# Kernel optimization log

Measured on AMD Instinct MI355X. Metric: run time of the kernel, lower is better.

## Reference

```python
import jax, jax.numpy as jnp
import numpy as np

B, D_IN, D_HID, D_OUT = 16384, 512, 512, 512
E, K = 8, 2
VQ_COEFF, LB_COEFF = 0.05, 0.01
LOG100 = float(np.log(100.0))
LOG2 = float(np.log(2.0))


def _normalize(v):
    # torch F.normalize(dim=1): x / max(||x||, 1e-12)
    n = jnp.linalg.norm(v, axis=-1, keepdims=True)
    return v / jnp.maximum(n, 1e-12)


def _cv_squared(v):
    # torch .var() is unbiased (ddof=1)
    return jnp.var(v, ddof=1) / (jnp.mean(v) ** 2 + 1e-10)


def _rbm_layer(x, rm, W, b, ca, temp):
    # x: [B, d_in], rm: [E, d_in], W: [E, d_out, d_in], b: [E, d_out]
    rm_n = jax.lax.stop_gradient(_normalize(rm))          # .detach() in source
    nx = _normalize(x)
    dists = nx @ rm_n.T                                    # [B, E]
    top_v, top_i = jax.lax.top_k(dists, K)                 # [B, K]
    tv = jax.nn.softmax(top_v, axis=-1)                    # softmax over top-k
    bsz = dists.shape[0]
    attn = jnp.zeros_like(dists).at[jnp.arange(bsz)[:, None], top_i].set(tv)
    # const_attention is frozen (requires_grad=False)
    inp_att = jnp.exp(jnp.minimum(jax.lax.stop_gradient(ca), LOG100))  # [E]
    # dense gather-compute-scatter: expert e output for every token, masked by attn
    eo = jnp.einsum('bi,eoi->beo', x, W) * inp_att[None, :, None] + b[None, :, :]
    out = jnp.einsum('be,beo->bo', jax.lax.stop_gradient(attn), eo)    # att.detach()
    out = out * jnp.exp(jnp.minimum(temp, LOG100))
    # aux losses (eval mode: no EMA memory update)
    vq = -(nx[:, None, :] * rm_n[top_i]).sum(-1)           # [B, K]
    vq_loss = (tv * vq).sum(-1).mean()
    lb = _cv_squared(attn.sum(0))
    aux = VQ_COEFF * vq_loss + LB_COEFF * lb               # sim_coeff = 0
    return out, aux


def setup_inputs() -> dict:
    key = jax.random.key(0)
    ks = jax.random.split(key, 8)
    x = jax.random.normal(ks[0], (B, D_IN), dtype=jnp.float32)
    rm0 = _normalize(jax.random.normal(ks[1], (E, D_IN), dtype=jnp.float32))
    W0 = jax.random.normal(ks[2], (E, D_HID, D_IN), dtype=jnp.float32) / np.sqrt(D_IN)
    b0 = jnp.zeros((E, D_HID), dtype=jnp.float32)
    rm1 = _normalize(jax.random.normal(ks[3], (E, D_HID), dtype=jnp.float32))
    W1 = jax.random.normal(ks[4], (E, D_OUT, D_HID), dtype=jnp.float32) / np.sqrt(D_HID)
    b1 = jnp.zeros((E, D_OUT), dtype=jnp.float32)
    temp0 = jnp.full((1,), LOG2, dtype=jnp.float32)
    temp1 = jnp.full((1,), LOG2, dtype=jnp.float32)
    ca0 = jnp.zeros((E,), dtype=jnp.float32)
    ca1 = jnp.zeros((E,), dtype=jnp.float32)
    return {"x": x, "rm0": rm0, "W0": W0, "b0": b0, "temp0": temp0, "ca0": ca0,
            "rm1": rm1, "W1": W1, "b1": b1, "temp1": temp1, "ca1": ca1}


def reference(x, rm0, W0, b0, temp0, ca0, rm1, W1, b1, temp1, ca1):
    h0, a0 = _rbm_layer(x, rm0, W0, b0, ca0, temp0)
    h_emb = h0                      # embedding tapped after layer 0 (pre-activation)
    h = jax.nn.relu(h0)             # norm_type=None -> no norm
    h1, a1 = _rbm_layer(h, rm1, W1, b1, ca1, temp1)
    return (h_emb, h1, a0 + a1)
```

## Files before the change

kernel.cpp:

```cpp
#include <hip/hip_runtime.h>
#include <cmath>
#include <cstdint>

#define NTOK   16384
#define DM     512
#define NEXP   8
#define LOG100 4.605170185988092f

typedef _Float16 half8  __attribute__((ext_vector_type(8)));
typedef _Float16 half4  __attribute__((ext_vector_type(4)));
typedef float    floatx4 __attribute__((ext_vector_type(4)));

#define MFMA_F16(a, b, c) __builtin_amdgcn_mfma_f32_16x16x32_f16((a), (b), (c), 0, 0, 0)

__device__ __forceinline__ void gl_lds16(const void* g, void* l) {
    __builtin_amdgcn_global_load_lds(
        (const __attribute__((address_space(1))) void*)g,
        (__attribute__((address_space(3))) void*)l, 16, 0, 0);
}


__global__ __launch_bounds__(256) void prep_kernel(
    const float* __restrict__ rm0, const float* __restrict__ rm1,
    const float* __restrict__ ca0, const float* __restrict__ ca1,
    const float* __restrict__ temp0, const float* __restrict__ temp1,
    float* __restrict__ ctrl, float* __restrict__ rmn)
{
    int tid = threadIdx.x, lane = tid & 63, w = tid >> 6;
    if (tid < 32) ((int*)ctrl)[tid] = 0;
    if (tid >= 32 && tid < 48) ctrl[tid] = 0.f;
    if (tid == 48 || tid == 49) ctrl[tid] = 0.f;
    if (tid == 50) ctrl[50] = expf(fminf(temp0[0], LOG100));
    if (tid == 51) ctrl[51] = expf(fminf(temp1[0], LOG100));
    if (tid >= 52 && tid < 68) {
        int i = tid - 52;
        ctrl[tid] = expf(fminf(i < 8 ? ca0[i] : ca1[i - 8], LOG100));
    }
    for (int r = w; r < 16; r += 4) {
        const float* src = (r < 8) ? (rm0 + r * DM) : (rm1 + (r - 8) * DM);
        float v[8]; float ss = 0.f;
        #pragma unroll
        for (int j = 0; j < 8; ++j) { v[j] = src[lane + 64 * j]; ss += v[j] * v[j]; }
        #pragma unroll
        for (int off = 32; off > 0; off >>= 1) ss += __shfl_xor(ss, off);
        float inv = 1.f / fmaxf(sqrtf(ss), 1e-12f);
        float* dst = rmn + r * DM;
        #pragma unroll
        for (int j = 0; j < 8; ++j) dst[lane + 64 * j] = v[j] * inv;
    }
}

__global__ __launch_bounds__(256) void conv_w_kernel(
    const float4* __restrict__ W0, const float4* __restrict__ W1,
    half4* __restrict__ w0hi, half4* __restrict__ w0lo, half4* __restrict__ w1h)
{
    int i = blockIdx.x * 256 + threadIdx.x;
    float4 a = W0[i], b = W1[i];
    const float* ap = (const float*)&a;
    const float* bp = (const float*)&b;
    half4 hi, lo, h1;
    #pragma unroll
    for (int j = 0; j < 4; ++j) {
        _Float16 h = (_Float16)ap[j];
        hi[j] = h;
        lo[j] = (_Float16)(ap[j] - (float)h);
        h1[j] = (_Float16)bp[j];
    }
    w0hi[i] = hi; w0lo[i] = lo; w1h[i] = h1;
}

__global__ __launch_bounds__(256) void route_kernel(
    const float* __restrict__ src,
    const float* __restrict__ rmn,
    int relu_in,
    _Float16* __restrict__ dst_hi,
    _Float16* __restrict__ dst_lo,
    float* __restrict__ zbase,
    unsigned char* __restrict__ key,
    float2* __restrict__ wts,
    float2* __restrict__ bs)
{
    __shared__ float rmLds[NEXP * DM];
    int tid = threadIdx.x;
    for (int i = tid; i < NEXP * DM; i += 256) rmLds[i] = rmn[i];
    __syncthreads();
    int lane = tid & 63, w = tid >> 6;
    int token = blockIdx.x * 4 + w;

    const float* row = src + (size_t)token * DM;
    float x[8]; float ss = 0.f;
    #pragma unroll
    for (int j = 0; j < 8; ++j) {
        float v = row[lane + 64 * j];
        if (relu_in) v = fmaxf(v, 0.f);
        x[j] = v; ss += v * v;
    }
    #pragma unroll
    for (int j = 0; j < 8; ++j) {
        _Float16 h = (_Float16)x[j];
        dst_hi[(size_t)token * DM + lane + 64 * j] = h;
        if (dst_lo) dst_lo[(size_t)token * DM + lane + 64 * j] = (_Float16)(x[j] - (float)h);
    }
    {
        float4 z = make_float4(0.f, 0.f, 0.f, 0.f);
        float4* zr = (float4*)(zbase + (size_t)token * DM);
        zr[lane * 2] = z;
        zr[lane * 2 + 1] = z;
    }
    float d[8];
    #pragma unroll
    for (int e = 0; e < 8; ++e) {
        float a = 0.f;
        #pragma unroll
        for (int j = 0; j < 8; ++j) a += x[j] * rmLds[e * DM + lane + 64 * j];
        d[e] = a;
    }
    #pragma unroll
    for (int off = 32; off > 0; off >>= 1) {
        ss += __shfl_xor(ss, off);
        #pragma unroll
        for (int e = 0; e < 8; ++e) d[e] += __shfl_xor(d[e], off);
    }
    float inv = 1.f / fmaxf(sqrtf(ss), 1e-12f);
    float best = -1e30f, second = -1e30f; int be = 0, se = 0;
    #pragma unroll
    for (int e = 0; e < 8; ++e) {
        float de = d[e] * inv;
        if (de > best)        { second = best; se = be; best = de; be = e; }
        else if (de > second) { second = de; se = e; }
    }
    float z = expf(second - best);
    float w0 = 1.f / (1.f + z), w1 = z / (1.f + z);
    if (lane == 0) {
        key[token] = (unsigned char)be;
        key[NTOK + token] = (unsigned char)se;
        wts[token] = make_float2(w0, w1);
        bs[token] = make_float2(best, second);
    }
}

__global__ __launch_bounds__(256) void compact_kernel(
    const unsigned char* __restrict__ key,
    const float2* __restrict__ wts,
    const float2* __restrict__ bs,
    int* __restrict__ cnt,
    unsigned short* __restrict__ bkt,
    float* __restrict__ imp,
    float* __restrict__ vq_acc)
{
    int slot = blockIdx.x >> 3, e = blockIdx.x & 7;
    const unsigned char* k = key + slot * NTOK;
    unsigned short* ob = bkt + (size_t)(slot * 8 + e) * NTOK;
    __shared__ int wc[2][4];
    int tid = threadIdx.x, lane = tid & 63, w = tid >> 6;
    int base = 0;
    float wsum = 0.f, vqs = 0.f;
    for (int c = 0; c < 64; ++c) {
        int tok = c * 256 + tid;
        bool m = (k[tok] == (unsigned char)e);
        unsigned long long mask = __ballot(m);
        int p = c & 1;
        if (lane == 0) wc[p][w] = __popcll(mask);
        __syncthreads();
        int off = base;
        for (int i = 0; i < w; ++i) off += wc[p][i];
        if (m) {
            int pre = __popcll(mask & ((1ull << lane) - 1ull));
            ob[off + pre] = (unsigned short)tok;
            float2 wp = wts[tok]; float2 b2 = bs[tok];
            float wv = slot ? wp.y : wp.x;
            wsum += wv;
            vqs  += wv * (slot ? b2.y : b2.x);
        }
        base += wc[p][0] + wc[p][1] + wc[p][2] + wc[p][3];
    }
    #pragma unroll
    for (int off = 32; off > 0; off >>= 1) {
        wsum += __shfl_xor(wsum, off);
        vqs  += __shfl_xor(vqs, off);
    }
    __shared__ float rw[4], rv[4];
    if (lane == 0) { rw[w] = wsum; rv[w] = vqs; }
    __syncthreads();
    if (tid == 0) {
        cnt[slot * 8 + e] = base;
        float W = rw[0] + rw[1] + rw[2] + rw[3];
        float V = rv[0] + rv[1] + rv[2] + rv[3];
        atomicAdd(&imp[e], W);
        atomicAdd(vq_acc, -V);
    }
}

template <bool SPLIT>
__global__ __launch_bounds__(256) void gemm_kernel(
    const _Float16* __restrict__ Ahi, const _Float16* __restrict__ Alo,
    const _Float16* __restrict__ Whi, const _Float16* __restrict__ Wlo,
    const float* __restrict__ bias,
    const float* __restrict__ iav,
    const float* __restrict__ tscp,
    const int* __restrict__ cnt,
    const unsigned short* __restrict__ bkt,
    const float2* __restrict__ wts,
    float* __restrict__ outp)
{
    __shared__ __align__(16) _Float16 lds[2 * 128 * 64];
    __shared__ int tokLds[128];
    _Float16* tA = lds;
    _Float16* tB = lds + 128 * 64;

    int bx = blockIdx.x;
    int e = bx & 7; int r = bx >> 3;
    int n0 = (r & 3) << 7; r >>= 2;
    int slot = r & 1; int mt = r >> 1;
    int M = cnt[slot * 8 + e];
    int m0 = mt << 7;
    if (m0 >= M) return;
    int valid = min(128, M - m0);
    int tid = threadIdx.x, lane = tid & 63, w = tid >> 6;
    const unsigned short* ob = bkt + (size_t)(slot * 8 + e) * NTOK;
    if (tid < 128) tokLds[tid] = ob[m0 + min(tid, valid - 1)];
    __syncthreads();

    floatx4 acc[4][4];
    #pragma unroll
    for (int mi = 0; mi < 4; ++mi)
        #pragma unroll
        for (int ni = 0; ni < 4; ++ni) acc[mi][ni] = (floatx4){0.f, 0.f, 0.f, 0.f};

    const _Float16* WbH = Whi + ((size_t)e * DM + n0) * DM;
    const _Float16* WbL = SPLIT ? (Wlo + ((size_t)e * DM + n0) * DM) : nullptr;

    int subRow = lane >> 3, p = lane & 7;
    int cSt = p ^ (subRow & 7);
    int wm = w >> 1, wn = w & 1;
    int r0 = wm * 64, c0 = wn * 64;
    int q = lane >> 4, l15 = lane & 15;

    constexpr int KIT = SPLIT ? 16 : 8;
    constexpr int KSTEP = SPLIT ? 32 : 64;

    const _Float16* aPtr[4]; const _Float16* bPtr[4];
    _Float16* aDst[4]; _Float16* bDst[4];
    #pragma unroll
    for (int jj = 0; jj < 4; ++jj) {
        int j = w + jj * 4;
        int row = j * 8 + subRow;
        int tok = tokLds[row];
        if constexpr (SPLIT) {
            aPtr[jj] = (cSt < 4) ? (Ahi + (size_t)tok * DM + cSt * 8)
                                 : (Alo + (size_t)tok * DM + (cSt - 4) * 8);
            bPtr[jj] = (cSt < 4) ? (WbH + (size_t)row * DM + cSt * 8)
                                 : (WbL + (size_t)row * DM + (cSt - 4) * 8);
        } else {
            aPtr[jj] = Ahi + (size_t)tok * DM + cSt * 8;
            bPtr[jj] = WbH + (size_t)row * DM + cSt * 8;
        }
        aDst[jj] = tA + j * 512;
        bDst[jj] = tB + j * 512;
    }
    const half8 *aHp[4], *aLp[4], *bHp[4], *bLp[4];
    #pragma unroll
    for (int i = 0; i < 4; ++i) {
        int ra = r0 + i * 16 + l15;
        int rb = c0 + i * 16 + l15;
        if constexpr (SPLIT) {
            aHp[i] = (const half8*)(tA + ra * 64 + ((q) ^ (ra & 7)) * 8);
            aLp[i] = (const half8*)(tA + ra * 64 + ((q + 4) ^ (ra & 7)) * 8);
            bHp[i] = (const half8*)(tB + rb * 64 + ((q) ^ (rb & 7)) * 8);
            bLp[i] = (const half8*)(tB + rb * 64 + ((q + 4) ^ (rb & 7)) * 8);
        } else {
            aHp[i] = (const half8*)(tA + ra * 64 + ((q) ^ (ra & 7)) * 8);
            aLp[i] = (const half8*)(tA + ra * 64 + ((4 + q) ^ (ra & 7)) * 8);
            bHp[i] = (const half8*)(tB + rb * 64 + ((q) ^ (rb & 7)) * 8);
            bLp[i] = (const half8*)(tB + rb * 64 + ((4 + q) ^ (rb & 7)) * 8);
        }
    }

    for (int kb = 0; kb < KIT; ++kb) {
        #pragma unroll
        for (int jj = 0; jj < 4; ++jj) {
            gl_lds16(aPtr[jj], (void*)aDst[jj]);
            aPtr[jj] += KSTEP;
        }
        #pragma unroll
        for (int jj = 0; jj < 4; ++jj) {
            gl_lds16(bPtr[jj], (void*)bDst[jj]);
            bPtr[jj] += KSTEP;
        }
        __syncthreads();

        if constexpr (SPLIT) {
            half8 ah[4], al[4];
            #pragma unroll
            for (int mi = 0; mi < 4; ++mi) { ah[mi] = *aHp[mi]; al[mi] = *aLp[mi]; }
            #pragma unroll
            for (int ni = 0; ni < 4; ++ni) {
                half8 bh = *bHp[ni];
                half8 bl = *bLp[ni];
                #pragma unroll
                for (int mi = 0; mi < 4; ++mi) acc[mi][ni] = MFMA_F16(ah[mi], bh, acc[mi][ni]);
                #pragma unroll
                for (int mi = 0; mi < 4; ++mi) acc[mi][ni] = MFMA_F16(ah[mi], bl, acc[mi][ni]);
                #pragma unroll
                for (int mi = 0; mi < 4; ++mi) acc[mi][ni] = MFMA_F16(al[mi], bh, acc[mi][ni]);
            }
        } else {
            half8 a[4];
            #pragma unroll
            for (int mi = 0; mi < 4; ++mi) a[mi] = *aHp[mi];
            #pragma unroll
            for (int ni = 0; ni < 4; ++ni) {
                half8 b = *bHp[ni];
                #pragma unroll
                for (int mi = 0; mi < 4; ++mi) acc[mi][ni] = MFMA_F16(a[mi], b, acc[mi][ni]);
            }
            #pragma unroll
            for (int mi = 0; mi < 4; ++mi) a[mi] = *aLp[mi];
            #pragma unroll
            for (int ni = 0; ni < 4; ++ni) {
                half8 b = *bLp[ni];
                #pragma unroll
                for (int mi = 0; mi < 4; ++mi) acc[mi][ni] = MFMA_F16(a[mi], b, acc[mi][ni]);
            }
        }
        __syncthreads();
    }

    float t = *tscp, iae = iav[e];
    float bv[4];
    #pragma unroll
    for (int ni = 0; ni < 4; ++ni) bv[ni] = bias[e * DM + n0 + c0 + ni * 16 + l15];
    #pragma unroll
    for (int mi = 0; mi < 4; ++mi) {
        int liBase = r0 + mi * 16 + q * 4;
        #pragma unroll
        for (int reg = 0; reg < 4; ++reg) {
            int li = liBase + reg;
            if (li < valid) {
                int tok = tokLds[li];
                float2 wp = wts[tok];
                float wgt = slot ? wp.y : wp.x;
                float sg = t * wgt * iae, sb = t * wgt;
                float* orow = outp + (size_t)tok * DM + n0;
                #pragma unroll
                for (int ni = 0; ni < 4; ++ni) {
                    float v = acc[mi][ni][reg] * sg + bv[ni] * sb;
                    int c = c0 + ni * 16 + l15;
                    unsafeAtomicAdd(&orow[c], v);
                }
            }
        }
    }
}

__global__ void finalize_kernel(const float* __restrict__ ctrl, float* __restrict__ outp)
{
    if (threadIdx.x == 0) {
        float aux = 0.f;
        for (int l = 0; l < 2; ++l) {
            float vq = ctrl[48 + l] / (float)NTOK;
            float mean = 0.f;
            for (int e = 0; e < 8; ++e) mean += ctrl[32 + l * 8 + e];
            mean *= 0.125f;
            float s = 0.f;
            for (int e = 0; e < 8; ++e) {
                float d = ctrl[32 + l * 8 + e] - mean;
                s += d * d;
            }
            float var = s / 7.f;
            float lb = var / (mean * mean + 1e-10f);
            aux += 0.05f * vq + 0.01f * lb;
        }
        *outp = aux;
    }
}

extern "C" void kernel_launch(void* const* d_in, const int* in_sizes, int n_in,
                              void* d_out, int out_size, void* d_ws, size_t ws_size,
                              hipStream_t stream) {
    const float* x     = (const float*)d_in[0];
    const float* rm0   = (const float*)d_in[1];
    const float* W0    = (const float*)d_in[2];
    const float* b0    = (const float*)d_in[3];
    const float* temp0 = (const float*)d_in[4];
    const float* ca0   = (const float*)d_in[5];
    const float* rm1   = (const float*)d_in[6];
    const float* W1    = (const float*)d_in[7];
    const float* b1    = (const float*)d_in[8];
    const float* temp1 = (const float*)d_in[9];
    const float* ca1   = (const float*)d_in[10];
    float* out = (float*)d_out;

    char* ws = (char*)d_ws;
    float* ctrl = (float*)ws;
    int*   cnt  = (int*)ctrl;
    float* imp  = ctrl + 32;
    float* vq   = ctrl + 48;
    float* tsc  = ctrl + 50;
    float* ia   = ctrl + 52;
    float* rmn  = ctrl + 128;
    float2*        wts = (float2*)(ws + (size_t)64  * 1024);
    float2*        bs  = (float2*)(ws + (size_t)384 * 1024);
    unsigned char* key = (unsigned char*)(ws + (size_t)704 * 1024);

    char* big = ws + (1 << 20);
    half4*          w0hi4 = (half4*)(big);
    half4*          w0lo4 = (half4*)(big + (size_t)4  * 1024 * 1024);
    half4*          w1h4  = (half4*)(big + (size_t)8  * 1024 * 1024);
    _Float16*       w0hi  = (_Float16*)w0hi4;
    _Float16*       w0lo  = (_Float16*)w0lo4;
    _Float16*       w1h   = (_Float16*)w1h4;
    _Float16*       h16   = (_Float16*)(big + (size_t)12 * 1024 * 1024);
    unsigned short* bkt   = (unsigned short*)(big + (size_t)28 * 1024 * 1024);

    _Float16* xhi = (_Float16*)(out + (size_t)NTOK * DM);
    _Float16* xlo = xhi + (size_t)NTOK * DM;
    float* h0 = out;
    float* h1 = out + (size_t)NTOK * DM;

    prep_kernel<<<1, 256, 0, stream>>>(rm0, rm1, ca0, ca1, temp0, temp1, ctrl, rmn);
    conv_w_kernel<<<2048, 256, 0, stream>>>((const float4*)W0, (const float4*)W1,
                                            w0hi4, w0lo4, w1h4);

    route_kernel<<<4096, 256, 0, stream>>>(x, rmn, 0, xhi, xlo, h0,
        key, wts, bs);
    compact_kernel<<<16, 256, 0, stream>>>(key, wts, bs, cnt, bkt, imp, vq);
    gemm_kernel<true><<<8192, 256, 0, stream>>>(xhi, xlo, w0hi, w0lo, b0, ia, tsc,
        cnt, bkt, wts, h0);

    route_kernel<<<4096, 256, 0, stream>>>(h0, rmn + 4096, 1, h16, (_Float16*)nullptr, h1,
        key + 2 * NTOK, wts + NTOK, bs + NTOK);
    compact_kernel<<<16, 256, 0, stream>>>(key + 2 * NTOK, wts + NTOK, bs + NTOK,
        cnt + 16, bkt + 16 * NTOK, imp + 8, vq + 1);
    gemm_kernel<false><<<8192, 256, 0, stream>>>(h16, (const _Float16*)nullptr, w1h,
        (const _Float16*)nullptr, b1, ia + 8, tsc + 1,
        cnt + 16, bkt + 16 * NTOK, wts + NTOK, h1);

    finalize_kernel<<<1, 64, 0, stream>>>(ctrl, out + (size_t)2 * NTOK * DM);
}
```

Measured before the change: 509.4 us.

## Fuse fp16 conversion into gathered GEMMs and replace atomics with slot-separated stores

The first routing kernel no longer writes fp16 hi/lo copies of x or zero-fills the output. The layer-0 GEMM now loads fp32 token rows directly, splits them into hi/lo halves in registers, and writes each top-k slot's result to its own buffer with plain stores. The second routing pass sums the two slot buffers into the embedding output and applies relu in the same pass. The layer-1 GEMM converts relu'd fp32 input on the fly and runs as two ordered launches, one per slot, with the second accumulating non-atomically. Tiles shrink from 128x128 to 64x64, which means many more blocks and more redundant weight reloads, in exchange for removing the atomic-add traffic and the intermediate fp16 buffers.

```diff
diff --git a/kernel.cpp b/kernel.cpp
--- a/kernel.cpp
+++ b/kernel.cpp
@@ -69,16 +69,9 @@
     w0hi[i] = hi; w0lo[i] = lo; w1h[i] = h1;
 }
 
-__global__ __launch_bounds__(256) void route_kernel(
-    const float* __restrict__ src,
-    const float* __restrict__ rmn,
-    int relu_in,
-    _Float16* __restrict__ dst_hi,
-    _Float16* __restrict__ dst_lo,
-    float* __restrict__ zbase,
-    unsigned char* __restrict__ key,
-    float2* __restrict__ wts,
-    float2* __restrict__ bs)
+__global__ __launch_bounds__(256) void route0_kernel(
+    const float* __restrict__ src, const float* __restrict__ rmn,
+    unsigned char* __restrict__ key, float2* __restrict__ wts, float2* __restrict__ bs)
 {
     __shared__ float rmLds[NEXP * DM];
     int tid = threadIdx.x;
@@ -90,23 +83,7 @@
     const float* row = src + (size_t)token * DM;
     float x[8]; float ss = 0.f;
     #pragma unroll
-    for (int j = 0; j < 8; ++j) {
-        float v = row[lane + 64 * j];
-        if (relu_in) v = fmaxf(v, 0.f);
-        x[j] = v; ss += v * v;
-    }
-    #pragma unroll
-    for (int j = 0; j < 8; ++j) {
-        _Float16 h = (_Float16)x[j];
-        dst_hi[(size_t)token * DM + lane + 64 * j] = h;
-        if (dst_lo) dst_lo[(size_t)token * DM + lane + 64 * j] = (_Float16)(x[j] - (float)h);
-    }
-    {
-        float4 z = make_float4(0.f, 0.f, 0.f, 0.f);
-        float4* zr = (float4*)(zbase + (size_t)token * DM);
-        zr[lane * 2] = z;
-        zr[lane * 2 + 1] = z;
-    }
+    for (int j = 0; j < 8; ++j) { float v = row[lane + 64 * j]; x[j] = v; ss += v * v; }
     float d[8];
     #pragma unroll
     for (int e = 0; e < 8; ++e) {
@@ -139,14 +116,63 @@
     }
 }
 
+__global__ __launch_bounds__(256) void route1_kernel(
+    const float* s0, const float* s1, float* hemb,
+    const float* __restrict__ rmn,
+    unsigned char* __restrict__ key, float2* __restrict__ wts, float2* __restrict__ bs)
+{
+    __shared__ float rmLds[NEXP * DM];
+    int tid = threadIdx.x;
+    for (int i = tid; i < NEXP * DM; i += 256) rmLds[i] = rmn[i];
+    __syncthreads();
+    int lane = tid & 63, w = tid >> 6;
+    int token = blockIdx.x * 4 + w;
+
+    float x[8]; float ss = 0.f;
+    #pragma unroll
+    for (int j = 0; j < 8; ++j) {
+        size_t idx = (size_t)token * DM + lane + 64 * j;
+        float v = s0[idx] + s1[idx];
+        hemb[idx] = v;
+        float r = fmaxf(v, 0.f);
+        x[j] = r; ss += r * r;
+    }
+    float d[8];
+    #pragma unroll
+    for (int e = 0; e < 8; ++e) {
+        float a = 0.f;
+        #pragma unroll
+        for (int j = 0; j < 8; ++j) a += x[j] * rmLds[e * DM + lane + 64 * j];
+        d[e] = a;
+    }
+    #pragma unroll
+    for (int off = 32; off > 0; off >>= 1) {
+        ss += __shfl_xor(ss, off);
+        #pragma unroll
+        for (int e = 0; e < 8; ++e) d[e] += __shfl_xor(d[e], off);
+    }
+    float inv = 1.f / fmaxf(sqrtf(ss), 1e-12f);
+    float best = -1e30f, second = -1e30f; int be = 0, se = 0;
+    #pragma unroll
+    for (int e = 0; e < 8; ++e) {
+        float de = d[e] * inv;
+        if (de > best)        { second = best; se = be; best = de; be = e; }
+        else if (de > second) { second = de; se = e; }
+    }
+    float z = expf(second - best);
+    float w0 = 1.f / (1.f + z), w1 = z / (1.f + z);
+    if (lane == 0) {
+        key[token] = (unsigned char)be;
+        key[NTOK + token] = (unsigned char)se;
+        wts[token] = make_float2(w0, w1);
+        bs[token] = make_float2(best, second);
+    }
+}
+
 __global__ __launch_bounds__(256) void compact_kernel(
-    const unsigned char* __restrict__ key,
-    const float2* __restrict__ wts,
-    const float2* __restrict__ bs,
-    int* __restrict__ cnt,
-    unsigned short* __restrict__ bkt,
-    float* __restrict__ imp,
-    float* __restrict__ vq_acc)
+    const unsigned char* __restrict__ key, const float2* __restrict__ wts,
+    const float2* __restrict__ bs, int* __restrict__ cnt,
+    unsigned short* __restrict__ bkt, float* __restrict__ imp, float* __restrict__ vq_acc)
 {
     int slot = blockIdx.x >> 3, e = blockIdx.x & 7;
     const unsigned char* k = key + slot * NTOK;
@@ -184,154 +210,247 @@
     __syncthreads();
     if (tid == 0) {
         cnt[slot * 8 + e] = base;
-        float W = rw[0] + rw[1] + rw[2] + rw[3];
-        float V = rv[0] + rv[1] + rv[2] + rv[3];
-        atomicAdd(&imp[e], W);
-        atomicAdd(vq_acc, -V);
-    }
-}
-
-template <bool SPLIT>
-__global__ __launch_bounds__(256) void gemm_kernel(
-    const _Float16* __restrict__ Ahi, const _Float16* __restrict__ Alo,
+        atomicAdd(&imp[e], rw[0] + rw[1] + rw[2] + rw[3]);
+        atomicAdd(vq_acc, -(rv[0] + rv[1] + rv[2] + rv[3]));
+    }
+}
+
+__global__ __launch_bounds__(256) void gemm0_kernel(
+    const float* __restrict__ x,
     const _Float16* __restrict__ Whi, const _Float16* __restrict__ Wlo,
-    const float* __restrict__ bias,
-    const float* __restrict__ iav,
+    const float* __restrict__ bias, const float* __restrict__ iav,
     const float* __restrict__ tscp,
-    const int* __restrict__ cnt,
-    const unsigned short* __restrict__ bkt,
+    const int* __restrict__ cnt, const unsigned short* __restrict__ bkt,
     const float2* __restrict__ wts,
-    float* __restrict__ outp)
-{
-    __shared__ __align__(16) _Float16 lds[2 * 128 * 64];
-    __shared__ int tokLds[128];
-    _Float16* tA = lds;
-    _Float16* tB = lds + 128 * 64;
+    float* __restrict__ s0, float* __restrict__ s1)
+{
+    __shared__ __align__(16) _Float16 tA[64 * 64];
+    __shared__ __align__(16) _Float16 tB[64 * 64];
+    __shared__ int tokLds[64];
 
     int bx = blockIdx.x;
-    int e = bx & 7; int r = bx >> 3;
-    int n0 = (r & 3) << 7; r >>= 2;
-    int slot = r & 1; int mt = r >> 1;
+    int e = bx & 7, nIdx = (bx >> 3) & 7, slot = (bx >> 6) & 1, mt = bx >> 7;
     int M = cnt[slot * 8 + e];
-    int m0 = mt << 7;
+    int m0 = mt << 6;
     if (m0 >= M) return;
-    int valid = min(128, M - m0);
+    int n0 = nIdx << 6;
+    int valid = min(64, M - m0);
     int tid = threadIdx.x, lane = tid & 63, w = tid >> 6;
     const unsigned short* ob = bkt + (size_t)(slot * 8 + e) * NTOK;
-    if (tid < 128) tokLds[tid] = ob[m0 + min(tid, valid - 1)];
+    if (tid < 64) tokLds[tid] = ob[m0 + min(tid, valid - 1)];
     __syncthreads();
 
-    floatx4 acc[4][4];
-    #pragma unroll
-    for (int mi = 0; mi < 4; ++mi)
-        #pragma unroll
-        for (int ni = 0; ni < 4; ++ni) acc[mi][ni] = (floatx4){0.f, 0.f, 0.f, 0.f};
+    floatx4 acc[2][2];
+    #pragma unroll
+    for (int mi = 0; mi < 2; ++mi)
+        #pragma unroll
+        for (int ni = 0; ni < 2; ++ni) acc[mi][ni] = (floatx4){0.f, 0.f, 0.f, 0.f};
 
     const _Float16* WbH = Whi + ((size_t)e * DM + n0) * DM;
-    const _Float16* WbL = SPLIT ? (Wlo + ((size_t)e * DM + n0) * DM) : nullptr;
+    const _Float16* WbL = Wlo + ((size_t)e * DM + n0) * DM;
 
     int subRow = lane >> 3, p = lane & 7;
     int cSt = p ^ (subRow & 7);
-    int wm = w >> 1, wn = w & 1;
-    int r0 = wm * 64, c0 = wn * 64;
-    int q = lane >> 4, l15 = lane & 15;
-
-    constexpr int KIT = SPLIT ? 16 : 8;
-    constexpr int KSTEP = SPLIT ? 32 : 64;
-
-    const _Float16* aPtr[4]; const _Float16* bPtr[4];
-    _Float16* aDst[4]; _Float16* bDst[4];
-    #pragma unroll
-    for (int jj = 0; jj < 4; ++jj) {
+    const _Float16* bPtr[2]; _Float16* bDst[2];
+    #pragma unroll
+    for (int jj = 0; jj < 2; ++jj) {
         int j = w + jj * 4;
         int row = j * 8 + subRow;
-        int tok = tokLds[row];
-        if constexpr (SPLIT) {
-            aPtr[jj] = (cSt < 4) ? (Ahi + (size_t)tok * DM + cSt * 8)
-                                 : (Alo + (size_t)tok * DM + (cSt - 4) * 8);
-            bPtr[jj] = (cSt < 4) ? (WbH + (size_t)row * DM + cSt * 8)
-                                 : (WbL + (size_t)row * DM + (cSt - 4) * 8);
-        } else {
-            aPtr[jj] = Ahi + (size_t)tok * DM + cSt * 8;
-            bPtr[jj] = WbH + (size_t)row * DM + cSt * 8;
-        }
-        aDst[jj] = tA + j * 512;
+        bPtr[jj] = (cSt < 4) ? (WbH + (size_t)row * DM + cSt * 8)
+                             : (WbL + (size_t)row * DM + (cSt - 4) * 8);
         bDst[jj] = tB + j * 512;
     }
-    const half8 *aHp[4], *aLp[4], *bHp[4], *bLp[4];
-    #pragma unroll
-    for (int i = 0; i < 4; ++i) {
+    int ar = tid >> 2, kc = tid & 3;
+    const float4* aBase = (const float4*)(x + (size_t)tokLds[ar] * DM);
+    _Float16* aDstHi = tA + ar * 64 + ((kc)     ^ (ar & 7)) * 8;
+    _Float16* aDstLo = tA + ar * 64 + ((kc + 4) ^ (ar & 7)) * 8;
+
+    int wm = w >> 1, wn = w & 1;
+    int r0 = wm * 32, c0 = wn * 32;
+    int q = lane >> 4, l15 = lane & 15;
+    const half8 *aHp[2], *aLp[2], *bHp[2], *bLp[2];
+    #pragma unroll
+    for (int i = 0; i < 2; ++i) {
         int ra = r0 + i * 16 + l15;
+        aHp[i] = (const half8*)(tA + ra * 64 + ((q)     ^ (ra & 7)) * 8);
+        aLp[i] = (const half8*)(tA + ra * 64 + ((q + 4) ^ (ra & 7)) * 8);
         int rb = c0 + i * 16 + l15;
-        if constexpr (SPLIT) {
-            aHp[i] = (const half8*)(tA + ra * 64 + ((q) ^ (ra & 7)) * 8);
-            aLp[i] = (const half8*)(tA + ra * 64 + ((q + 4) ^ (ra & 7)) * 8);
-            bHp[i] = (const half8*)(tB + rb * 64 + ((q) ^ (rb & 7)) * 8);
-            bLp[i] = (const half8*)(tB + rb * 64 + ((q + 4) ^ (rb & 7)) * 8);
-        } else {
-            aHp[i] = (const half8*)(tA + ra * 64 + ((q) ^ (ra & 7)) * 8);
-            aLp[i] = (const half8*)(tA + ra * 64 + ((4 + q) ^ (ra & 7)) * 8);
-            bHp[i] = (const half8*)(tB + rb * 64 + ((q) ^ (rb & 7)) * 8);
-            bLp[i] = (const half8*)(tB + rb * 64 + ((4 + q) ^ (rb & 7)) * 8);
-        }
-    }
-
-    for (int kb = 0; kb < KIT; ++kb) {
-        #pragma unroll
-        for (int jj = 0; jj < 4; ++jj) {
-            gl_lds16(aPtr[jj], (void*)aDst[jj]);
-            aPtr[jj] += KSTEP;
-        }
-        #pragma unroll
-        for (int jj = 0; jj < 4; ++jj) {
-            gl_lds16(bPtr[jj], (void*)bDst[jj]);
-            bPtr[jj] += KSTEP;
-        }
+        bHp[i] = (const half8*)(tB + rb * 64 + ((q)     ^ (rb & 7)) * 8);
+        bLp[i] = (const half8*)(tB + rb * 64 + ((q + 4) ^ (rb & 7)) * 8);
+    }
+
+    float4 pf0 = aBase[kc * 2], pf1 = aBase[kc * 2 + 1];
+    for (int kb = 0; kb < 16; ++kb) {
+        float fv[8] = {pf0.x, pf0.y, pf0.z, pf0.w, pf1.x, pf1.y, pf1.z, pf1.w};
+        half8 hi, lo;
+        #pragma unroll
+        for (int j = 0; j < 8; ++j) {
+            _Float16 h = (_Float16)fv[j];
+            hi[j] = h;
+            lo[j] = (_Float16)(fv[j] - (float)h);
+        }
+        *(half8*)aDstHi = hi;
+        *(half8*)aDstLo = lo;
+        gl_lds16(bPtr[0], (void*)bDst[0]);
+        gl_lds16(bPtr[1], (void*)bDst[1]);
+        bPtr[0] += 32; bPtr[1] += 32;
         __syncthreads();
-
-        if constexpr (SPLIT) {
-            half8 ah[4], al[4];
+        if (kb + 1 < 16) {
+            int idx = (kb + 1) * 8 + kc * 2;
+            pf0 = aBase[idx]; pf1 = aBase[idx + 1];
+        }
+        half8 ah[2], al[2];
+        #pragma unroll
+        for (int mi = 0; mi < 2; ++mi) { ah[mi] = *aHp[mi]; al[mi] = *aLp[mi]; }
+        #pragma unroll
+        for (int ni = 0; ni < 2; ++ni) {
+            half8 bh = *bHp[ni];
+            half8 bl = *bLp[ni];
             #pragma unroll
-            for (int mi = 0; mi < 4; ++mi) { ah[mi] = *aHp[mi]; al[mi] = *aLp[mi]; }
+            for (int mi = 0; mi < 2; ++mi) acc[mi][ni] = MFMA_F16(ah[mi], bh, acc[mi][ni]);
             #pragma unroll
-            for (int ni = 0; ni < 4; ++ni) {
-                half8 bh = *bHp[ni];
-                half8 bl = *bLp[ni];
+            for (int mi = 0; mi < 2; ++mi) acc[mi][ni] = MFMA_F16(ah[mi], bl, acc[mi][ni]);
+            #pragma unroll
+            for (int mi = 0; mi < 2; ++mi) acc[mi][ni] = MFMA_F16(al[mi], bh, acc[mi][ni]);
+        }
+        __syncthreads();
+    }
+
+    float* sOut = slot ? s1 : s0;
+    float t = *tscp, iae = iav[e];
+    float bv[2];
+    #pragma unroll
+    for (int ni = 0; ni < 2; ++ni) bv[ni] = bias[e * DM + n0 + c0 + ni * 16 + l15];
+    #pragma unroll
+    for (int mi = 0; mi < 2; ++mi) {
+        int liBase = r0 + mi * 16 + q * 4;
+        #pragma unroll
+        for (int reg = 0; reg < 4; ++reg) {
+            int li = liBase + reg;
+            if (li < valid) {
+                int tok = tokLds[li];
+                float2 wp = wts[tok];
+                float wgt = slot ? wp.y : wp.x;
+                float sg = t * wgt * iae, sb = t * wgt;
+                float* orow = sOut + (size_t)tok * DM + n0;
                 #pragma unroll
-                for (int mi = 0; mi < 4; ++mi) acc[mi][ni] = MFMA_F16(ah[mi], bh, acc[mi][ni]);
-                #pragma unroll
-                for (int mi = 0; mi < 4; ++mi) acc[mi][ni] = MFMA_F16(ah[mi], bl, acc[mi][ni]);
-                #pragma unroll
-                for (int mi = 0; mi < 4; ++mi) acc[mi][ni] = MFMA_F16(al[mi], bh, acc[mi][ni]);
+                for (int ni = 0; ni < 2; ++ni)
+                    orow[c0 + ni * 16 + l15] = acc[mi][ni][reg] * sg + bv[ni] * sb;
             }
-        } else {
-            half8 a[4];
+        }
+    }
+}
+
+__global__ __launch_bounds__(256) void gemm1_kernel(
+    const float* __restrict__ hsrc,
+    const _Float16* __restrict__ Wh,
+    const float* __restrict__ bias, const float* __restrict__ iav,
+    const float* __restrict__ tscp,
+    const int* __restrict__ cnt, const unsigned short* __restrict__ bkt,
+    const float2* __restrict__ wts,
+    int slot, int accum,
+    float* __restrict__ outp)
+{
+    __shared__ __align__(16) _Float16 tA[64 * 64];
+    __shared__ __align__(16) _Float16 tB[64 * 64];
+    __shared__ int tokLds[64];
+
+    int bx = blockIdx.x;
+    int e = bx & 7, nIdx = (bx >> 3) & 7, mt = bx >> 6;
+    int M = cnt[slot * 8 + e];
+    int m0 = mt << 6;
+    if (m0 >= M) return;
+    int n0 = nIdx << 6;
+    int valid = min(64, M - m0);
+    int tid = threadIdx.x, lane = tid & 63, w = tid >> 6;
+    const unsigned short* ob = bkt + (size_t)(slot * 8 + e) * NTOK;
+    if (tid < 64) tokLds[tid] = ob[m0 + min(tid, valid - 1)];
+    __syncthreads();
+
+    floatx4 acc[2][2];
+    #pragma unroll
+    for (int mi = 0; mi < 2; ++mi)
+        #pragma unroll
+        for (int ni = 0; ni < 2; ++ni) acc[mi][ni] = (floatx4){0.f, 0.f, 0.f, 0.f};
+
+    const _Float16* Wb = Wh + ((size_t)e * DM + n0) * DM;
+
+    int subRow = lane >> 3, p = lane & 7;
+    int cSt = p ^ (subRow & 7);
+    const _Float16* bPtr[2]; _Float16* bDst[2];
+    #pragma unroll
+    for (int jj = 0; jj < 2; ++jj) {
+        int j = w + jj * 4;
+        int row = j * 8 + subRow;
+        bPtr[jj] = Wb + (size_t)row * DM + cSt * 8;
+        bDst[jj] = tB + j * 512;
+    }
+    int ar = tid >> 2, kc2 = (tid & 3) * 2;
+    const float4* aBase = (const float4*)(hsrc + (size_t)tokLds[ar] * DM);
+    _Float16* aDst0 = tA + ar * 64 + ((kc2)     ^ (ar & 7)) * 8;
+    _Float16* aDst1 = tA + ar * 64 + ((kc2 + 1) ^ (ar & 7)) * 8;
+
+    int wm = w >> 1, wn = w & 1;
+    int r0 = wm * 32, c0 = wn * 32;
+    int q = lane >> 4, l15 = lane & 15;
+    const half8 *aP0[2], *aP1[2], *bP0[2], *bP1[2];
+    #pragma unroll
+    for (int i = 0; i < 2; ++i) {
+        int ra = r0 + i * 16 + l15;
+        aP0[i] = (const half8*)(tA + ra * 64 + ((q)     ^ (ra & 7)) * 8);
+        aP1[i] = (const half8*)(tA + ra * 64 + ((4 + q) ^ (ra & 7)) * 8);
+        int rb = c0 + i * 16 + l15;
+        bP0[i] = (const half8*)(tB + rb * 64 + ((q)     ^ (rb & 7)) * 8);
+        bP1[i] = (const half8*)(tB + rb * 64 + ((4 + q) ^ (rb & 7)) * 8);
+    }
+
+    float4 pf[4];
+    #pragma unroll
+    for (int j = 0; j < 4; ++j) pf[j] = aBase[kc2 * 2 + j];
+    for (int kb = 0; kb < 8; ++kb) {
+        const float* fp = (const float*)pf;
+        half8 h0v, h1v;
+        #pragma unroll
+        for (int j = 0; j < 8; ++j) h0v[j] = (_Float16)fmaxf(fp[j], 0.f);
+        #pragma unroll
+        for (int j = 0; j < 8; ++j) h1v[j] = (_Float16)fmaxf(fp[8 + j], 0.f);
+        *(half8*)aDst0 = h0v;
+        *(half8*)aDst1 = h1v;
+        gl_lds16(bPtr[0], (void*)bDst[0]);
+        gl_lds16(bPtr[1], (void*)bDst[1]);
+        bPtr[0] += 64; bPtr[1] += 64;
+        __syncthreads();
+        if (kb + 1 < 8) {
+            int idx = (kb + 1) * 16 + kc2 * 2;
             #pragma unroll
-            for (int mi = 0; mi < 4; ++mi) a[mi] = *aHp[mi];
+            for (int j = 0; j < 4; ++j) pf[j] = aBase[idx + j];
+        }
+        half8 a[2];
+        #pragma unroll
+        for (int mi = 0; mi < 2; ++mi) a[mi] = *aP0[mi];
+        #pragma unroll
+        for (int ni = 0; ni < 2; ++ni) {
+            half8 b = *bP0[ni];
             #pragma unroll
-            for (int ni = 0; ni < 4; ++ni) {
-                half8 b = *bHp[ni];
-                #pragma unroll
-                for (int mi = 0; mi < 4; ++mi) acc[mi][ni] = MFMA_F16(a[mi], b, acc[mi][ni]);
-            }
+            for (int mi = 0; mi < 2; ++mi) acc[mi][ni] = MFMA_F16(a[mi], b, acc[mi][ni]);
+        }
+        #pragma unroll
+        for (int mi = 0; mi < 2; ++mi) a[mi] = *aP1[mi];
+        #pragma unroll
+        for (int ni = 0; ni < 2; ++ni) {
+            half8 b = *bP1[ni];
             #pragma unroll
-            for (int mi = 0; mi < 4; ++mi) a[mi] = *aLp[mi];
-            #pragma unroll
-            for (int ni = 0; ni < 4; ++ni) {
-                half8 b = *bLp[ni];
-                #pragma unroll
-                for (int mi = 0; mi < 4; ++mi) acc[mi][ni] = MFMA_F16(a[mi], b, acc[mi][ni]);
-            }
+            for (int mi = 0; mi < 2; ++mi) acc[mi][ni] = MFMA_F16(a[mi], b, acc[mi][ni]);
         }
         __syncthreads();
     }
 
     float t = *tscp, iae = iav[e];
-    float bv[4];
-    #pragma unroll
-    for (int ni = 0; ni < 4; ++ni) bv[ni] = bias[e * DM + n0 + c0 + ni * 16 + l15];
-    #pragma unroll
-    for (int mi = 0; mi < 4; ++mi) {
+    float bv[2];
+    #pragma unroll
+    for (int ni = 0; ni < 2; ++ni) bv[ni] = bias[e * DM + n0 + c0 + ni * 16 + l15];
+    #pragma unroll
+    for (int mi = 0; mi < 2; ++mi) {
         int liBase = r0 + mi * 16 + q * 4;
         #pragma unroll
         for (int reg = 0; reg < 4; ++reg) {
@@ -343,10 +462,10 @@
                 float sg = t * wgt * iae, sb = t * wgt;
                 float* orow = outp + (size_t)tok * DM + n0;
                 #pragma unroll
-                for (int ni = 0; ni < 4; ++ni) {
+                for (int ni = 0; ni < 2; ++ni) {
                     float v = acc[mi][ni][reg] * sg + bv[ni] * sb;
                     int c = c0 + ni * 16 + l15;
-                    unsafeAtomicAdd(&orow[c], v);
+                    if (accum) orow[c] += v; else orow[c] = v;
                 }
             }
         }
@@ -410,31 +529,28 @@
     _Float16*       w0hi  = (_Float16*)w0hi4;
     _Float16*       w0lo  = (_Float16*)w0lo4;
     _Float16*       w1h   = (_Float16*)w1h4;
-    _Float16*       h16   = (_Float16*)(big + (size_t)12 * 1024 * 1024);
-    unsigned short* bkt   = (unsigned short*)(big + (size_t)28 * 1024 * 1024);
-
-    _Float16* xhi = (_Float16*)(out + (size_t)NTOK * DM);
-    _Float16* xlo = xhi + (size_t)NTOK * DM;
-    float* h0 = out;
-    float* h1 = out + (size_t)NTOK * DM;
+    unsigned short* bkt   = (unsigned short*)(big + (size_t)12 * 1024 * 1024);
+
+    float* s0 = out;
+    float* s1 = out + (size_t)NTOK * DM;
 
     prep_kernel<<<1, 256, 0, stream>>>(rm0, rm1, ca0, ca1, temp0, temp1, ctrl, rmn);
     conv_w_kernel<<<2048, 256, 0, stream>>>((const float4*)W0, (const float4*)W1,
                                             w0hi4, w0lo4, w1h4);
 
-    route_kernel<<<4096, 256, 0, stream>>>(x, rmn, 0, xhi, xlo, h0,
-        key, wts, bs);
+    route0_kernel<<<4096, 256, 0, stream>>>(x, rmn, key, wts, bs);
     compact_kernel<<<16, 256, 0, stream>>>(key, wts, bs, cnt, bkt, imp, vq);
-    gemm_kernel<true><<<8192, 256, 0, stream>>>(xhi, xlo, w0hi, w0lo, b0, ia, tsc,
-        cnt, bkt, wts, h0);
-
-    route_kernel<<<4096, 256, 0, stream>>>(h0, rmn + 4096, 1, h16, (_Float16*)nullptr, h1,
+    gemm0_kernel<<<32768, 256, 0, stream>>>(x, w0hi, w0lo, b0, ia, tsc,
+        cnt, bkt, wts, s0, s1);
+
+    route1_kernel<<<4096, 256, 0, stream>>>(s0, s1, s0, rmn + 4096,
         key + 2 * NTOK, wts + NTOK, bs + NTOK);
     compact_kernel<<<16, 256, 0, stream>>>(key + 2 * NTOK, wts + NTOK, bs + NTOK,
         cnt + 16, bkt + 16 * NTOK, imp + 8, vq + 1);
-    gemm_kernel<false><<<8192, 256, 0, stream>>>(h16, (const _Float16*)nullptr, w1h,
-        (const _Float16*)nullptr, b1, ia + 8, tsc + 1,
-        cnt + 16, bkt + 16 * NTOK, wts + NTOK, h1);
+    gemm1_kernel<<<16384, 256, 0, stream>>>(s0, w1h, b1, ia + 8, tsc + 1,
+        cnt + 16, bkt + 16 * NTOK, wts + NTOK, 0, 0, s1);
+    gemm1_kernel<<<16384, 256, 0, stream>>>(s0, w1h, b1, ia + 8, tsc + 1,
+        cnt + 16, bkt + 16 * NTOK, wts + NTOK, 1, 1, s1);
 
     finalize_kernel<<<1, 64, 0, stream>>>(ctrl, out + (size_t)2 * NTOK * DM);
 }
```

After: 507.0 us. About the same (-0.5%).
